# Optimization experiments

Hardware: AMD Instinct MI355X
Metric: run time of the kernel (lower is better)

The kernel has to match this reference:

```python
import jax, jax.numpy as jnp
import numpy as np

GROUP_SIZE = 64
SHARED_EXPERT_WEIGHT = 1.0
# FP4 E2M1 codebook: sign bit + {0,.5,1,1.5,2,3,4,6}
FP4_TABLE = jnp.array([0.0, 0.5, 1.0, 1.5, 2.0, 3.0, 4.0, 6.0,
                       -0.0, -0.5, -1.0, -1.5, -2.0, -3.0, -4.0, -6.0], dtype=jnp.float32)


def dequant_fp4(packed, scales, group_size=GROUP_SIZE):
    """packed: [..., K//8, N] int32 (8 nibbles along K per word),
    scales: [..., K//group_size, N] -> dequantized [..., K, N] fp32."""
    shifts = (jnp.arange(8, dtype=jnp.int32) * 4)[:, None]          # [8,1]
    nib = jnp.right_shift(packed[..., :, None, :], shifts) & 0xF     # [..., K//8, 8, N]
    w = FP4_TABLE[nib]
    K = packed.shape[-2] * 8
    w = w.reshape(packed.shape[:-2] + (K, packed.shape[-1]))         # [..., K, N]
    s = jnp.repeat(scales, group_size, axis=-2)                      # [..., K, N]
    return w * s


def setup_inputs() -> dict:
    key = jax.random.key(0)
    ks = jax.random.split(key, 12)
    T, K, I, E, TOPK = 2048, 2048, 1024, 8, 2
    GS = GROUP_SIZE
    MAXI = 2**31 - 1
    u = lambda k, shp: jax.random.uniform(k, shp, jnp.float32, 0.005, 0.02)
    probs = jax.random.uniform(ks[10], (T, TOPK), jnp.float32)
    probs = probs / probs.sum(-1, keepdims=True)
    return {
        "hidden_states": jax.random.normal(ks[0], (T, K), jnp.float32),
        "gate_up_weight_packed": jax.random.randint(ks[1], (E, K // 8, 2 * I), 0, MAXI, jnp.int32),
        "gate_up_scales": u(ks[2], (E, K // GS, 2 * I)),
        "down_weight_packed": jax.random.randint(ks[3], (E, I // 8, K), 0, MAXI, jnp.int32),
        "down_scales": u(ks[4], (E, I // GS, K)),
        "shared_gate_up_packed": jax.random.randint(ks[5], (K // 8, 2 * I), 0, MAXI, jnp.int32),
        "shared_gate_up_scales": u(ks[6], (K // GS, 2 * I)),
        "shared_down_packed": jax.random.randint(ks[7], (I // 8, K), 0, MAXI, jnp.int32),
        "shared_down_scales": u(ks[8], (I // GS, K)),
        "expert_ids": jax.random.randint(ks[9], (T, TOPK), 0, E, jnp.int32),
        "expert_probs": probs,
    }


def reference(hidden_states, gate_up_weight_packed, gate_up_scales,
              down_weight_packed, down_scales,
              shared_gate_up_packed, shared_gate_up_scales,
              shared_down_packed, shared_down_scales,
              expert_ids, expert_probs):
    x = hidden_states                                                # [T, K]
    E = gate_up_weight_packed.shape[0]
    # --- routed experts: dequant + grouped GEMM over all tokens per expert ---
    Wgu = dequant_fp4(gate_up_weight_packed, gate_up_scales)         # [E, K, 2I]
    Wd = dequant_fp4(down_weight_packed, down_scales)                # [E, I, K]
    h = jnp.einsum('tk,ekn->etn', x, Wgu)                            # [E, T, 2I]
    gate, up = jnp.split(h, 2, axis=-1)
    act = jax.nn.silu(gate) * up                                     # [E, T, I]
    y = jnp.einsum('eti,eik->etk', act, Wd)                          # [E, T, K]
    # combine[t,e] = sum over top-k slots routed to e of prob
    one_hot = jax.nn.one_hot(expert_ids, E, dtype=x.dtype)           # [T, topk, E]
    combine = jnp.einsum('tk,tke->te', expert_probs, one_hot)        # [T, E]
    out = jnp.einsum('te,etk->tk', combine, y)                       # [T, K]
    # --- shared expert (always applied, weighted) ---
    Wgu_s = dequant_fp4(shared_gate_up_packed, shared_gate_up_scales)  # [K, 2I]
    Wd_s = dequant_fp4(shared_down_packed, shared_down_scales)         # [I, K]
    hs = x @ Wgu_s
    gs, us = jnp.split(hs, 2, axis=-1)
    shared_out = (jax.nn.silu(gs) * us) @ Wd_s
    return out + SHARED_EXPERT_WEIGHT * shared_out
```

## Files before the change

### kernel.cpp

```cpp
#include <hip/hip_runtime.h>
#include <hip/hip_bf16.h>

#define T_TOK 2048
#define K_DIM 2048
#define I_DIM 1024
#define NE    8
#define TOPK  2
#define GS    64

#define NSLOT  (T_TOK * TOPK)
#define TOTROW (NSLOT + T_TOK)
#define MAXITEM 32

typedef __attribute__((ext_vector_type(8))) short short8;
typedef __attribute__((ext_vector_type(4))) float f32x4;

#define WS_XB   ((size_t)65536)
#define WS_ACT  (WS_XB  + (size_t)2048 * 2048 * 2)
#define WS_Y    (WS_ACT + (size_t)TOTROW * 1024 * 2)


__device__ __forceinline__ unsigned pack2(float a, float b) {
    __hip_bfloat162 h = __float22bfloat162_rn(make_float2(a, b));
    return *reinterpret_cast<unsigned*>(&h);
}

__device__ __forceinline__ unsigned scale2(unsigned p, float s) {
    float f0 = __uint_as_float(p << 16) * s;
    float f1 = __uint_as_float(p & 0xFFFF0000u) * s;
    return pack2(f0, f1);
}

__device__ __forceinline__ float bf2f(ushort h) {
    return __uint_as_float((unsigned)h << 16);
}

__device__ __forceinline__ void dq_word(unsigned w, float s, unsigned o[4]) {
    unsigned lo  = w & 0x0F0F0F0Fu;
    unsigned hi  = (w >> 4) & 0x0F0F0F0Fu;
    unsigned mlo = lo & 0x07070707u, mhi = hi & 0x07070707u;
    unsigned Hlo = __builtin_amdgcn_perm(0x40404040u, 0x3F3F3F00u, mlo);
    unsigned Hhi = __builtin_amdgcn_perm(0x40404040u, 0x3F3F3F00u, mhi);
    unsigned Llo = __builtin_amdgcn_perm(0xC0804000u, 0xC0800000u, mlo);
    unsigned Lhi = __builtin_amdgcn_perm(0xC0804000u, 0xC0800000u, mhi);
    Hlo |= (lo & 0x08080808u) << 4;
    Hhi |= (hi & 0x08080808u) << 4;
    unsigned e01 = __builtin_amdgcn_perm(Hlo, Llo, 0x05010400u);
    unsigned e23 = __builtin_amdgcn_perm(Hlo, Llo, 0x07030602u);
    unsigned o01 = __builtin_amdgcn_perm(Hhi, Lhi, 0x05010400u);
    unsigned o23 = __builtin_amdgcn_perm(Hhi, Lhi, 0x07030602u);
    o[0] = scale2(e01, s); o[1] = scale2(e23, s);
    o[2] = scale2(o01, s); o[3] = scale2(o23, s);
}

__device__ __forceinline__ void gld16(const void* g, void* l) {
    __builtin_amdgcn_global_load_lds(
        (const __attribute__((address_space(1))) unsigned*)g,
        (__attribute__((address_space(3))) unsigned*)l, 16, 0, 0);
}

#define PREP_BLK 2048
#define FRONT_GRID (PREP_BLK + 1)

__global__ __launch_bounds__(256) void k_front(
        const float* __restrict__ x, ushort* __restrict__ xb,
        const int* __restrict__ eids,
        int* __restrict__ gcnt, int* __restrict__ gbase,
        int* __restrict__ tileCnt, int* __restrict__ tileE, int* __restrict__ tileM,
        int* __restrict__ tok, int* __restrict__ inv) {
    int id = blockIdx.x;
    int tid = threadIdx.x;

    if (id < PREP_BLK) {
        int idx = id * 256 + tid;
        const float4* p = (const float4*)(x + (size_t)idx * 8);
        float4 f0 = p[0], f1 = p[1];
        unsigned u0 = pack2(f0.x, f0.z);
        unsigned u1 = pack2(f1.x, f1.z);
        unsigned u2 = pack2(f0.y, f0.w);
        unsigned u3 = pack2(f1.y, f1.w);
        *(int4*)(xb + (size_t)idx * 8) = make_int4(u0, u1, u2, u3);
    } else {
        __shared__ int lcnt[NE], lbase[NE], lcur[NE];
        if (tid < NE) lcnt[tid] = 0;
        __syncthreads();
        for (int i = tid; i < NSLOT; i += 256)
            atomicAdd(&lcnt[eids[i]], 1);
        __syncthreads();
        if (tid == 0) {
            int acc = 0;
            for (int e = 0; e < NE; e++) { lbase[e] = acc; acc += lcnt[e]; }
        }
        __syncthreads();
        if (tid < NE) lcur[tid] = lbase[tid];
        __syncthreads();
        for (int i = tid; i < NSLOT; i += 256) {
            int e = eids[i];
            int pos = atomicAdd(&lcur[e], 1);
            tok[pos] = i >> 1;
            inv[i] = pos;
        }
        for (int t = tid; t < T_TOK; t += 256)
            tok[NSLOT + t] = t;
        if (tid < NE) { gcnt[tid] = lcnt[tid]; gbase[tid] = lbase[tid]; }
        if (tid == 0) {
            gcnt[NE] = T_TOK; gbase[NE] = NSLOT;
            int nt = 0;
            for (int e = 0; e < NE + 1; e++) {
                int c = (e < NE) ? lcnt[e] : T_TOK;
                for (int m = 0; m < c; m += 256) { tileE[nt] = e; tileM[nt] = m; nt++; }
            }
            *tileCnt = nt;
            for (int i = nt; i < 64; i++) { tileE[i] = 0; tileM[i] = 0; }
        }
    }
}

__global__ __launch_bounds__(1024) void k_gemm_gateup(
        const ushort* __restrict__ xb,
        const int* __restrict__ gup, const float* __restrict__ gus,
        const int* __restrict__ sup, const float* __restrict__ sus,
        const int* __restrict__ gcnt, const int* __restrict__ gbase,
        const int* __restrict__ tileCnt, const int* __restrict__ tileE,
        const int* __restrict__ tileM,
        const int* __restrict__ tokid, ushort* __restrict__ act) {
    int item = blockIdx.y;
    if (item >= *tileCnt) return;
    int tid = threadIdx.x;
    int e = tileE[item], m0 = tileM[item];
    int cnt = gcnt[e], base = gbase[e];
    int n0 = blockIdx.x * 128;
    const int* wp; const float* sc;
    if (e < NE) { wp = gup + (size_t)e * 256 * 2048; sc = gus + (size_t)e * 32 * 2048; }
    else        { wp = sup; sc = sus; }

    __shared__ __align__(16) ushort xs[256 * 64];
    __shared__ __align__(16) ushort bs[256 * 64];

    int lane = tid & 63, wv = tid >> 6;
    int lid = lane & 15, quad = lane >> 4;
    int wr = wv >> 2, wc = wv & 3;
    int l8 = lane >> 3, l7 = lane & 7;
    int chunk = (l7 ^ l8) * 8;

    const ushort* aSrc[2];
    #pragma unroll
    for (int it = 0; it < 2; it++) {
        int rA = wv * 16 + it * 8 + l8;
        int t = (m0 + rA < cnt) ? tokid[base + m0 + rA] : 0;
        aSrc[it] = xb + (size_t)t * K_DIM + chunk;
    }

    int nloc = tid & 255;
    int kw0 = (tid >> 8) * 2;
    int bj = nloc & 63, bh = nloc >> 6;
    int ncol = (bj < 32) ? (n0 + bh * 32 + bj) : (I_DIM + n0 + bh * 32 + (bj - 32));
    ushort* bd0 = &bs[nloc * 64 + ((kw0    ) ^ (nloc & 7)) * 8];
    ushort* bd1 = &bs[nloc * 64 + ((kw0 + 1) ^ (nloc & 7)) * 8];

    float s   = sc[ncol];
    unsigned w0 = (unsigned)wp[(size_t)(kw0    ) * 2048 + ncol];
    unsigned w1 = (unsigned)wp[(size_t)(kw0 + 1) * 2048 + ncol];

    f32x4 acc[4][4] = {};

    for (int k0 = 0; k0 < K_DIM; k0 += 64) {
        #pragma unroll
        for (int it = 0; it < 2; it++)
            gld16(aSrc[it] + k0, &xs[(wv * 2 + it) * 512]);
        {
            unsigned o[4];
            dq_word(w0, s, o);
            *(int4*)bd0 = make_int4(o[0], o[1], o[2], o[3]);
            dq_word(w1, s, o);
            *(int4*)bd1 = make_int4(o[0], o[1], o[2], o[3]);
        }
        int kn = k0 + 64;
        if (kn < K_DIM) {
            s  = sc[(size_t)(kn >> 6) * 2048 + ncol];
            w0 = (unsigned)wp[(size_t)((kn >> 3) + kw0    ) * 2048 + ncol];
            w1 = (unsigned)wp[(size_t)((kn >> 3) + kw0 + 1) * 2048 + ncol];
        }
        __syncthreads();
        #pragma unroll
        for (int ks = 0; ks < 2; ks++) {
            int slot = ((ks * 4 + quad) ^ l7) * 8;
            short8 a[4], b[4];
            #pragma unroll
            for (int mt = 0; mt < 4; mt++)
                a[mt] = *(const short8*)&xs[(wr * 64 + mt * 16 + lid) * 64 + slot];
            #pragma unroll
            for (int nt = 0; nt < 4; nt++)
                b[nt] = *(const short8*)&bs[(wc * 64 + nt * 16 + lid) * 64 + slot];
            #pragma unroll
            for (int mt = 0; mt < 4; mt++)
                #pragma unroll
                for (int nt = 0; nt < 4; nt++)
                    acc[mt][nt] = __builtin_amdgcn_mfma_f32_16x16x32_bf16(
                        a[mt], b[nt], acc[mt][nt], 0, 0, 0);
        }
        __syncthreads();
    }

    int c7 = lid & 7;
    int delta = ((c7 >> 1) + ((c7 & 1) << 2)) - c7;
    #pragma unroll
    for (int mt = 0; mt < 4; mt++) {
        #pragma unroll
        for (int i = 0; i < 4; i++) {
            int row = wr * 64 + mt * 16 + quad * 4 + i;
            if (m0 + row < cnt) {
                size_t p = (size_t)(base + m0 + row);
                #pragma unroll
                for (int nt = 0; nt < 2; nt++) {
                    float g = acc[mt][nt][i], u = acc[mt][nt + 2][i];
                    float vv = g / (1.f + __expf(-g)) * u;
                    int ncol2 = n0 + wc * 32 + nt * 16 + lid;
                    __hip_bfloat16 hb = __float2bfloat16(vv);
                    act[p * I_DIM + ncol2 + delta] = *reinterpret_cast<ushort*>(&hb);
                }
            }
        }
    }
}

__global__ __launch_bounds__(1024) void k_gemm_down(
        const ushort* __restrict__ actb,
        const int* __restrict__ dwp, const float* __restrict__ dsc,
        const int* __restrict__ sdp, const float* __restrict__ sds,
        const int* __restrict__ gcnt, const int* __restrict__ gbase,
        const int* __restrict__ tileCnt, const int* __restrict__ tileE,
        const int* __restrict__ tileM,
        ushort* __restrict__ y) {
    int item = blockIdx.y;
    if (item >= *tileCnt) return;
    int tid = threadIdx.x;
    int e = tileE[item], m0 = tileM[item];
    int cnt = gcnt[e], base = gbase[e];
    int n0 = blockIdx.x * 256;
    const int* wp; const float* sc;
    if (e < NE) { wp = dwp + (size_t)e * 128 * 2048; sc = dsc + (size_t)e * 16 * 2048; }
    else        { wp = sdp; sc = sds; }

    __shared__ __align__(16) ushort xs[256 * 64];
    __shared__ __align__(16) ushort bs[256 * 64];

    int lane = tid & 63, wv = tid >> 6;
    int lid = lane & 15, quad = lane >> 4;
    int wr = wv >> 2, wc = wv & 3;
    int l8 = lane >> 3, l7 = lane & 7;
    int chunk = (l7 ^ l8) * 8;

    const ushort* aSrc[2];
    #pragma unroll
    for (int it = 0; it < 2; it++) {
        int rA = wv * 16 + it * 8 + l8;
        int rr = m0 + rA; if (rr >= cnt) rr = cnt - 1;
        aSrc[it] = actb + (size_t)(base + rr) * I_DIM + chunk;
    }

    int nloc = tid & 255;
    int kw0 = (tid >> 8) * 2;
    int ncol = n0 + nloc;
    ushort* bd0 = &bs[nloc * 64 + ((kw0    ) ^ (nloc & 7)) * 8];
    ushort* bd1 = &bs[nloc * 64 + ((kw0 + 1) ^ (nloc & 7)) * 8];

    float s   = sc[ncol];
    unsigned w0 = (unsigned)wp[(size_t)(kw0    ) * 2048 + ncol];
    unsigned w1 = (unsigned)wp[(size_t)(kw0 + 1) * 2048 + ncol];

    f32x4 acc[4][4] = {};

    for (int i0 = 0; i0 < I_DIM; i0 += 64) {
        #pragma unroll
        for (int it = 0; it < 2; it++)
            gld16(aSrc[it] + i0, &xs[(wv * 2 + it) * 512]);
        {
            unsigned o[4];
            dq_word(w0, s, o);
            *(int4*)bd0 = make_int4(o[0], o[1], o[2], o[3]);
            dq_word(w1, s, o);
            *(int4*)bd1 = make_int4(o[0], o[1], o[2], o[3]);
        }
        int in0 = i0 + 64;
        if (in0 < I_DIM) {
            s  = sc[(size_t)(in0 >> 6) * 2048 + ncol];
            w0 = (unsigned)wp[(size_t)((in0 >> 3) + kw0    ) * 2048 + ncol];
            w1 = (unsigned)wp[(size_t)((in0 >> 3) + kw0 + 1) * 2048 + ncol];
        }
        __syncthreads();
        #pragma unroll
        for (int ks = 0; ks < 2; ks++) {
            int slot = ((ks * 4 + quad) ^ l7) * 8;
            short8 a[4], b[4];
            #pragma unroll
            for (int mt = 0; mt < 4; mt++)
                a[mt] = *(const short8*)&xs[(wr * 64 + mt * 16 + lid) * 64 + slot];
            #pragma unroll
            for (int nt = 0; nt < 4; nt++)
                b[nt] = *(const short8*)&bs[(wc * 64 + nt * 16 + lid) * 64 + slot];
            #pragma unroll
            for (int mt = 0; mt < 4; mt++)
                #pragma unroll
                for (int nt = 0; nt < 4; nt++)
                    acc[mt][nt] = __builtin_amdgcn_mfma_f32_16x16x32_bf16(
                        a[mt], b[nt], acc[mt][nt], 0, 0, 0);
        }
        __syncthreads();
    }

    #pragma unroll
    for (int mt = 0; mt < 4; mt++) {
        #pragma unroll
        for (int i = 0; i < 4; i++) {
            int row = wr * 64 + mt * 16 + quad * 4 + i;
            if (m0 + row < cnt) {
                ushort* yrow = y + (size_t)(base + m0 + row) * 2048 + n0 + wc * 64 + lid;
                #pragma unroll
                for (int nt = 0; nt < 4; nt++) {
                    __hip_bfloat16 hb = __float2bfloat16(acc[mt][nt][i]);
                    yrow[nt * 16] = *reinterpret_cast<ushort*>(&hb);
                }
            }
        }
    }
}

__global__ __launch_bounds__(256) void k_combine(
        const ushort* __restrict__ y, const int* __restrict__ inv,
        const float* __restrict__ prb, float* __restrict__ out) {
    int idx = blockIdx.x * 256 + threadIdx.x;
    int t = idx >> 8;
    int c = (idx & 255) * 8;
    int p0 = inv[2 * t], p1 = inv[2 * t + 1];
    float w0 = prb[2 * t], w1 = prb[2 * t + 1];
    int4 a = *(const int4*)(y + (size_t)p0 * 2048 + c);
    int4 b = *(const int4*)(y + (size_t)p1 * 2048 + c);
    int4 s = *(const int4*)(y + (size_t)(NSLOT + t) * 2048 + c);
    const ushort* au = (const ushort*)&a;
    const ushort* bu = (const ushort*)&b;
    const ushort* su = (const ushort*)&s;
    float o[8];
    #pragma unroll
    for (int j = 0; j < 8; j++)
        o[j] = w0 * bf2f(au[j]) + w1 * bf2f(bu[j]) + bf2f(su[j]);
    *(float4*)(out + (size_t)t * 2048 + c)     = *(float4*)&o[0];
    *(float4*)(out + (size_t)t * 2048 + c + 4) = *(float4*)&o[4];
}

extern "C" void kernel_launch(void* const* d_in, const int* in_sizes, int n_in,
                              void* d_out, int out_size, void* d_ws, size_t ws_size,
                              hipStream_t stream) {
    const float* x    = (const float*)d_in[0];
    const int*   gup  = (const int*)d_in[1];
    const float* gus  = (const float*)d_in[2];
    const int*   dwp  = (const int*)d_in[3];
    const float* dsc  = (const float*)d_in[4];
    const int*   sup  = (const int*)d_in[5];
    const float* sus  = (const float*)d_in[6];
    const int*   sdp  = (const int*)d_in[7];
    const float* sds  = (const float*)d_in[8];
    const int*   eids = (const int*)d_in[9];
    const float* prb  = (const float*)d_in[10];
    float* out = (float*)d_out;

    char*   ws      = (char*)d_ws;
    int*    gcnt    = (int*)(ws + 0);
    int*    gbase   = (int*)(ws + 64);
    int*    tileCnt = (int*)(ws + 128);
    int*    tileE   = (int*)(ws + 192);
    int*    tileM   = (int*)(ws + 448);
    int*    tok     = (int*)(ws + 1024);
    int*    inv     = (int*)(ws + 25600);
    ushort* xb      = (ushort*)(ws + WS_XB);
    ushort* act     = (ushort*)(ws + WS_ACT);
    ushort* y       = (ushort*)(ws + WS_Y);

    k_front<<<FRONT_GRID, 256, 0, stream>>>(
        x, xb, eids, gcnt, gbase, tileCnt, tileE, tileM, tok, inv);
    k_gemm_gateup<<<dim3(I_DIM / 128, MAXITEM), 1024, 0, stream>>>(
        xb, gup, gus, sup, sus, gcnt, gbase, tileCnt, tileE, tileM, tok, act);
    k_gemm_down<<<dim3(K_DIM / 256, MAXITEM), 1024, 0, stream>>>(
        act, dwp, dsc, sdp, sds, gcnt, gbase, tileCnt, tileE, tileM, y);
    k_combine<<<(T_TOK * K_DIM / 8) / 256, 256, 0, stream>>>(y, inv, prb, out);
}
```

Before: 242.7 us.

## Double-buffer LDS tiles in gate-up and down GEMMs with one barrier per step

Result: faster. 232.4 us (-4.2%).

```diff
diff --git a/kernel.cpp b/kernel.cpp
--- a/kernel.cpp
+++ b/kernel.cpp
@@ -134,8 +134,8 @@
     if (e < NE) { wp = gup + (size_t)e * 256 * 2048; sc = gus + (size_t)e * 32 * 2048; }
     else        { wp = sup; sc = sus; }
 
-    __shared__ __align__(16) ushort xs[256 * 64];
-    __shared__ __align__(16) ushort bs[256 * 64];
+    __shared__ __align__(16) ushort xs[2][256 * 64];
+    __shared__ __align__(16) ushort bs[2][256 * 64];
 
     int lane = tid & 63, wv = tid >> 6;
     int lid = lane & 15, quad = lane >> 4;
@@ -155,43 +155,57 @@
     int kw0 = (tid >> 8) * 2;
     int bj = nloc & 63, bh = nloc >> 6;
     int ncol = (bj < 32) ? (n0 + bh * 32 + bj) : (I_DIM + n0 + bh * 32 + (bj - 32));
-    ushort* bd0 = &bs[nloc * 64 + ((kw0    ) ^ (nloc & 7)) * 8];
-    ushort* bd1 = &bs[nloc * 64 + ((kw0 + 1) ^ (nloc & 7)) * 8];
-
+    int bd0 = nloc * 64 + ((kw0    ) ^ (nloc & 7)) * 8;
+    int bd1 = nloc * 64 + ((kw0 + 1) ^ (nloc & 7)) * 8;
+
+    const int NT = K_DIM / 64;
+
+    #pragma unroll
+    for (int it = 0; it < 2; it++)
+        gld16(aSrc[it], &xs[0][(wv * 2 + it) * 512]);
     float s   = sc[ncol];
     unsigned w0 = (unsigned)wp[(size_t)(kw0    ) * 2048 + ncol];
     unsigned w1 = (unsigned)wp[(size_t)(kw0 + 1) * 2048 + ncol];
+    {
+        unsigned o[4];
+        dq_word(w0, s, o); *(int4*)&bs[0][bd0] = make_int4(o[0], o[1], o[2], o[3]);
+        dq_word(w1, s, o); *(int4*)&bs[0][bd1] = make_int4(o[0], o[1], o[2], o[3]);
+    }
+    s  = sc[(size_t)2048 + ncol];
+    w0 = (unsigned)wp[(size_t)(8 + kw0    ) * 2048 + ncol];
+    w1 = (unsigned)wp[(size_t)(8 + kw0 + 1) * 2048 + ncol];
+    __syncthreads();
 
     f32x4 acc[4][4] = {};
-
-    for (int k0 = 0; k0 < K_DIM; k0 += 64) {
-        #pragma unroll
-        for (int it = 0; it < 2; it++)
-            gld16(aSrc[it] + k0, &xs[(wv * 2 + it) * 512]);
-        {
+    int pp = 0;
+
+    #pragma unroll 2
+    for (int t = 0; t < NT; ++t) {
+        int nx = pp ^ 1;
+        if (t + 1 < NT) {
+            #pragma unroll
+            for (int it = 0; it < 2; it++)
+                gld16(aSrc[it] + (t + 1) * 64, &xs[nx][(wv * 2 + it) * 512]);
             unsigned o[4];
-            dq_word(w0, s, o);
-            *(int4*)bd0 = make_int4(o[0], o[1], o[2], o[3]);
-            dq_word(w1, s, o);
-            *(int4*)bd1 = make_int4(o[0], o[1], o[2], o[3]);
-        }
-        int kn = k0 + 64;
-        if (kn < K_DIM) {
-            s  = sc[(size_t)(kn >> 6) * 2048 + ncol];
-            w0 = (unsigned)wp[(size_t)((kn >> 3) + kw0    ) * 2048 + ncol];
-            w1 = (unsigned)wp[(size_t)((kn >> 3) + kw0 + 1) * 2048 + ncol];
-        }
-        __syncthreads();
+            dq_word(w0, s, o); *(int4*)&bs[nx][bd0] = make_int4(o[0], o[1], o[2], o[3]);
+            dq_word(w1, s, o); *(int4*)&bs[nx][bd1] = make_int4(o[0], o[1], o[2], o[3]);
+            if (t + 2 < NT) {
+                s  = sc[(size_t)(t + 2) * 2048 + ncol];
+                w0 = (unsigned)wp[(size_t)((t + 2) * 8 + kw0    ) * 2048 + ncol];
+                w1 = (unsigned)wp[(size_t)((t + 2) * 8 + kw0 + 1) * 2048 + ncol];
+            }
+        }
+        __builtin_amdgcn_s_setprio(1);
         #pragma unroll
         for (int ks = 0; ks < 2; ks++) {
             int slot = ((ks * 4 + quad) ^ l7) * 8;
             short8 a[4], b[4];
             #pragma unroll
             for (int mt = 0; mt < 4; mt++)
-                a[mt] = *(const short8*)&xs[(wr * 64 + mt * 16 + lid) * 64 + slot];
+                a[mt] = *(const short8*)&xs[pp][(wr * 64 + mt * 16 + lid) * 64 + slot];
             #pragma unroll
             for (int nt = 0; nt < 4; nt++)
-                b[nt] = *(const short8*)&bs[(wc * 64 + nt * 16 + lid) * 64 + slot];
+                b[nt] = *(const short8*)&bs[pp][(wc * 64 + nt * 16 + lid) * 64 + slot];
             #pragma unroll
             for (int mt = 0; mt < 4; mt++)
                 #pragma unroll
@@ -199,7 +213,9 @@
                     acc[mt][nt] = __builtin_amdgcn_mfma_f32_16x16x32_bf16(
                         a[mt], b[nt], acc[mt][nt], 0, 0, 0);
         }
-        __syncthreads();
+        __builtin_amdgcn_s_setprio(0);
+        __syncthreads();
+        pp = nx;
     }
 
     int c7 = lid & 7;
@@ -242,8 +258,8 @@
     if (e < NE) { wp = dwp + (size_t)e * 128 * 2048; sc = dsc + (size_t)e * 16 * 2048; }
     else        { wp = sdp; sc = sds; }
 
-    __shared__ __align__(16) ushort xs[256 * 64];
-    __shared__ __align__(16) ushort bs[256 * 64];
+    __shared__ __align__(16) ushort xs[2][256 * 64];
+    __shared__ __align__(16) ushort bs[2][256 * 64];
 
     int lane = tid & 63, wv = tid >> 6;
     int lid = lane & 15, quad = lane >> 4;
@@ -262,43 +278,57 @@
     int nloc = tid & 255;
     int kw0 = (tid >> 8) * 2;
     int ncol = n0 + nloc;
-    ushort* bd0 = &bs[nloc * 64 + ((kw0    ) ^ (nloc & 7)) * 8];
-    ushort* bd1 = &bs[nloc * 64 + ((kw0 + 1) ^ (nloc & 7)) * 8];
-
+    int bd0 = nloc * 64 + ((kw0    ) ^ (nloc & 7)) * 8;
+    int bd1 = nloc * 64 + ((kw0 + 1) ^ (nloc & 7)) * 8;
+
+    const int NT = I_DIM / 64;
+
+    #pragma unroll
+    for (int it = 0; it < 2; it++)
+        gld16(aSrc[it], &xs[0][(wv * 2 + it) * 512]);
     float s   = sc[ncol];
     unsigned w0 = (unsigned)wp[(size_t)(kw0    ) * 2048 + ncol];
     unsigned w1 = (unsigned)wp[(size_t)(kw0 + 1) * 2048 + ncol];
+    {
+        unsigned o[4];
+        dq_word(w0, s, o); *(int4*)&bs[0][bd0] = make_int4(o[0], o[1], o[2], o[3]);
+        dq_word(w1, s, o); *(int4*)&bs[0][bd1] = make_int4(o[0], o[1], o[2], o[3]);
+    }
+    s  = sc[(size_t)2048 + ncol];
+    w0 = (unsigned)wp[(size_t)(8 + kw0    ) * 2048 + ncol];
+    w1 = (unsigned)wp[(size_t)(8 + kw0 + 1) * 2048 + ncol];
+    __syncthreads();
 
     f32x4 acc[4][4] = {};
-
-    for (int i0 = 0; i0 < I_DIM; i0 += 64) {
-        #pragma unroll
-        for (int it = 0; it < 2; it++)
-            gld16(aSrc[it] + i0, &xs[(wv * 2 + it) * 512]);
-        {
+    int pp = 0;
+
+    #pragma unroll 2
+    for (int t = 0; t < NT; ++t) {
+        int nx = pp ^ 1;
+        if (t + 1 < NT) {
+            #pragma unroll
+            for (int it = 0; it < 2; it++)
+                gld16(aSrc[it] + (t + 1) * 64, &xs[nx][(wv * 2 + it) * 512]);
             unsigned o[4];
-            dq_word(w0, s, o);
-            *(int4*)bd0 = make_int4(o[0], o[1], o[2], o[3]);
-            dq_word(w1, s, o);
-            *(int4*)bd1 = make_int4(o[0], o[1], o[2], o[3]);
-        }
-        int in0 = i0 + 64;
-        if (in0 < I_DIM) {
-            s  = sc[(size_t)(in0 >> 6) * 2048 + ncol];
-            w0 = (unsigned)wp[(size_t)((in0 >> 3) + kw0    ) * 2048 + ncol];
-            w1 = (unsigned)wp[(size_t)((in0 >> 3) + kw0 + 1) * 2048 + ncol];
-        }
-        __syncthreads();
+            dq_word(w0, s, o); *(int4*)&bs[nx][bd0] = make_int4(o[0], o[1], o[2], o[3]);
+            dq_word(w1, s, o); *(int4*)&bs[nx][bd1] = make_int4(o[0], o[1], o[2], o[3]);
+            if (t + 2 < NT) {
+                s  = sc[(size_t)(t + 2) * 2048 + ncol];
+                w0 = (unsigned)wp[(size_t)((t + 2) * 8 + kw0    ) * 2048 + ncol];
+                w1 = (unsigned)wp[(size_t)((t + 2) * 8 + kw0 + 1) * 2048 + ncol];
+            }
+        }
+        __builtin_amdgcn_s_setprio(1);
         #pragma unroll
         for (int ks = 0; ks < 2; ks++) {
             int slot = ((ks * 4 + quad) ^ l7) * 8;
             short8 a[4], b[4];
             #pragma unroll
             for (int mt = 0; mt < 4; mt++)
-                a[mt] = *(const short8*)&xs[(wr * 64 + mt * 16 + lid) * 64 + slot];
+                a[mt] = *(const short8*)&xs[pp][(wr * 64 + mt * 16 + lid) * 64 + slot];
             #pragma unroll
             for (int nt = 0; nt < 4; nt++)
-                b[nt] = *(const short8*)&bs[(wc * 64 + nt * 16 + lid) * 64 + slot];
+                b[nt] = *(const short8*)&bs[pp][(wc * 64 + nt * 16 + lid) * 64 + slot];
             #pragma unroll
             for (int mt = 0; mt < 4; mt++)
                 #pragma unroll
@@ -306,7 +336,9 @@
                     acc[mt][nt] = __builtin_amdgcn_mfma_f32_16x16x32_bf16(
                         a[mt], b[nt], acc[mt][nt], 0, 0, 0);
         }
-        __syncthreads();
+        __builtin_amdgcn_s_setprio(0);
+        __syncthreads();
+        pp = nx;
     }
 
     #pragma unroll
```

## Halve GEMM N-tile and block size, add MFMA priority and pointer-increment loads

Applied to the files above, without the earlier changes.

Result: faster. 228.5 us (-5.9%).

```diff
diff --git a/kernel.cpp b/kernel.cpp
--- a/kernel.cpp
+++ b/kernel.cpp
@@ -116,7 +116,7 @@
     }
 }
 
-__global__ __launch_bounds__(1024) void k_gemm_gateup(
+__global__ __launch_bounds__(512) void k_gemm_gateup(
         const ushort* __restrict__ xb,
         const int* __restrict__ gup, const float* __restrict__ gus,
         const int* __restrict__ sup, const float* __restrict__ sus,
@@ -129,59 +129,64 @@
     int tid = threadIdx.x;
     int e = tileE[item], m0 = tileM[item];
     int cnt = gcnt[e], base = gbase[e];
-    int n0 = blockIdx.x * 128;
+    int n0 = blockIdx.x * 64;
     const int* wp; const float* sc;
     if (e < NE) { wp = gup + (size_t)e * 256 * 2048; sc = gus + (size_t)e * 32 * 2048; }
     else        { wp = sup; sc = sus; }
 
     __shared__ __align__(16) ushort xs[256 * 64];
-    __shared__ __align__(16) ushort bs[256 * 64];
+    __shared__ __align__(16) ushort bs[128 * 64];
 
     int lane = tid & 63, wv = tid >> 6;
     int lid = lane & 15, quad = lane >> 4;
-    int wr = wv >> 2, wc = wv & 3;
+    int wr = wv >> 1, wc = wv & 1;
     int l8 = lane >> 3, l7 = lane & 7;
     int chunk = (l7 ^ l8) * 8;
 
-    const ushort* aSrc[2];
-    #pragma unroll
-    for (int it = 0; it < 2; it++) {
-        int rA = wv * 16 + it * 8 + l8;
+    const ushort* aSrc[4];
+    #pragma unroll
+    for (int it = 0; it < 4; it++) {
+        int rA = wv * 32 + it * 8 + l8;
         int t = (m0 + rA < cnt) ? tokid[base + m0 + rA] : 0;
         aSrc[it] = xb + (size_t)t * K_DIM + chunk;
     }
 
-    int nloc = tid & 255;
-    int kw0 = (tid >> 8) * 2;
+    int nloc = tid & 127;
+    int kw0 = (tid >> 7) * 2;
     int bj = nloc & 63, bh = nloc >> 6;
     int ncol = (bj < 32) ? (n0 + bh * 32 + bj) : (I_DIM + n0 + bh * 32 + (bj - 32));
-    ushort* bd0 = &bs[nloc * 64 + ((kw0    ) ^ (nloc & 7)) * 8];
-    ushort* bd1 = &bs[nloc * 64 + ((kw0 + 1) ^ (nloc & 7)) * 8];
-
-    float s   = sc[ncol];
-    unsigned w0 = (unsigned)wp[(size_t)(kw0    ) * 2048 + ncol];
-    unsigned w1 = (unsigned)wp[(size_t)(kw0 + 1) * 2048 + ncol];
+    int bd0 = nloc * 64 + ((kw0    ) ^ (nloc & 7)) * 8;
+    int bd1 = nloc * 64 + ((kw0 + 1) ^ (nloc & 7)) * 8;
+
+    const int NT = K_DIM / 64;
+    const int* wq = wp + (size_t)kw0 * 2048 + ncol;
+    const float* sq = sc + ncol;
+    unsigned w0 = (unsigned)wq[0];
+    unsigned w1 = (unsigned)wq[2048];
+    float s = *sq;
+    wq += 16384; sq += 2048;
 
     f32x4 acc[4][4] = {};
 
-    for (int k0 = 0; k0 < K_DIM; k0 += 64) {
-        #pragma unroll
-        for (int it = 0; it < 2; it++)
-            gld16(aSrc[it] + k0, &xs[(wv * 2 + it) * 512]);
+    for (int t = 0; t < NT; ++t) {
+        #pragma unroll
+        for (int it = 0; it < 4; it++) {
+            gld16(aSrc[it], &xs[(wv * 4 + it) * 512]);
+            aSrc[it] += 64;
+        }
         {
             unsigned o[4];
-            dq_word(w0, s, o);
-            *(int4*)bd0 = make_int4(o[0], o[1], o[2], o[3]);
-            dq_word(w1, s, o);
-            *(int4*)bd1 = make_int4(o[0], o[1], o[2], o[3]);
-        }
-        int kn = k0 + 64;
-        if (kn < K_DIM) {
-            s  = sc[(size_t)(kn >> 6) * 2048 + ncol];
-            w0 = (unsigned)wp[(size_t)((kn >> 3) + kw0    ) * 2048 + ncol];
-            w1 = (unsigned)wp[(size_t)((kn >> 3) + kw0 + 1) * 2048 + ncol];
-        }
-        __syncthreads();
+            dq_word(w0, s, o); *(int4*)&bs[bd0] = make_int4(o[0], o[1], o[2], o[3]);
+            dq_word(w1, s, o); *(int4*)&bs[bd1] = make_int4(o[0], o[1], o[2], o[3]);
+        }
+        if (t + 1 < NT) {
+            w0 = (unsigned)wq[0];
+            w1 = (unsigned)wq[2048];
+            s = *sq;
+            wq += 16384; sq += 2048;
+        }
+        __syncthreads();
+        __builtin_amdgcn_s_setprio(1);
         #pragma unroll
         for (int ks = 0; ks < 2; ks++) {
             int slot = ((ks * 4 + quad) ^ l7) * 8;
@@ -199,6 +204,7 @@
                     acc[mt][nt] = __builtin_amdgcn_mfma_f32_16x16x32_bf16(
                         a[mt], b[nt], acc[mt][nt], 0, 0, 0);
         }
+        __builtin_amdgcn_s_setprio(0);
         __syncthreads();
     }
 
@@ -224,7 +230,7 @@
     }
 }
 
-__global__ __launch_bounds__(1024) void k_gemm_down(
+__global__ __launch_bounds__(512) void k_gemm_down(
         const ushort* __restrict__ actb,
         const int* __restrict__ dwp, const float* __restrict__ dsc,
         const int* __restrict__ sdp, const float* __restrict__ sds,
@@ -237,58 +243,63 @@
     int tid = threadIdx.x;
     int e = tileE[item], m0 = tileM[item];
     int cnt = gcnt[e], base = gbase[e];
-    int n0 = blockIdx.x * 256;
+    int n0 = blockIdx.x * 128;
     const int* wp; const float* sc;
     if (e < NE) { wp = dwp + (size_t)e * 128 * 2048; sc = dsc + (size_t)e * 16 * 2048; }
     else        { wp = sdp; sc = sds; }
 
     __shared__ __align__(16) ushort xs[256 * 64];
-    __shared__ __align__(16) ushort bs[256 * 64];
+    __shared__ __align__(16) ushort bs[128 * 64];
 
     int lane = tid & 63, wv = tid >> 6;
     int lid = lane & 15, quad = lane >> 4;
-    int wr = wv >> 2, wc = wv & 3;
+    int wr = wv >> 1, wc = wv & 1;
     int l8 = lane >> 3, l7 = lane & 7;
     int chunk = (l7 ^ l8) * 8;
 
-    const ushort* aSrc[2];
-    #pragma unroll
-    for (int it = 0; it < 2; it++) {
-        int rA = wv * 16 + it * 8 + l8;
+    const ushort* aSrc[4];
+    #pragma unroll
+    for (int it = 0; it < 4; it++) {
+        int rA = wv * 32 + it * 8 + l8;
         int rr = m0 + rA; if (rr >= cnt) rr = cnt - 1;
         aSrc[it] = actb + (size_t)(base + rr) * I_DIM + chunk;
     }
 
-    int nloc = tid & 255;
-    int kw0 = (tid >> 8) * 2;
+    int nloc = tid & 127;
+    int kw0 = (tid >> 7) * 2;
     int ncol = n0 + nloc;
-    ushort* bd0 = &bs[nloc * 64 + ((kw0    ) ^ (nloc & 7)) * 8];
-    ushort* bd1 = &bs[nloc * 64 + ((kw0 + 1) ^ (nloc & 7)) * 8];
-
-    float s   = sc[ncol];
-    unsigned w0 = (unsigned)wp[(size_t)(kw0    ) * 2048 + ncol];
-    unsigned w1 = (unsigned)wp[(size_t)(kw0 + 1) * 2048 + ncol];
+    int bd0 = nloc * 64 + ((kw0    ) ^ (nloc & 7)) * 8;
+    int bd1 = nloc * 64 + ((kw0 + 1) ^ (nloc & 7)) * 8;
+
+    const int NT = I_DIM / 64;
+    const int* wq = wp + (size_t)kw0 * 2048 + ncol;
+    const float* sq = sc + ncol;
+    unsigned w0 = (unsigned)wq[0];
+    unsigned w1 = (unsigned)wq[2048];
+    float s = *sq;
+    wq += 16384; sq += 2048;
 
     f32x4 acc[4][4] = {};
 
-    for (int i0 = 0; i0 < I_DIM; i0 += 64) {
-        #pragma unroll
-        for (int it = 0; it < 2; it++)
-            gld16(aSrc[it] + i0, &xs[(wv * 2 + it) * 512]);
+    for (int t = 0; t < NT; ++t) {
+        #pragma unroll
+        for (int it = 0; it < 4; it++) {
+            gld16(aSrc[it], &xs[(wv * 4 + it) * 512]);
+            aSrc[it] += 64;
+        }
         {
             unsigned o[4];
-            dq_word(w0, s, o);
-            *(int4*)bd0 = make_int4(o[0], o[1], o[2], o[3]);
-            dq_word(w1, s, o);
-            *(int4*)bd1 = make_int4(o[0], o[1], o[2], o[3]);
-        }
-        int in0 = i0 + 64;
-        if (in0 < I_DIM) {
-            s  = sc[(size_t)(in0 >> 6) * 2048 + ncol];
-            w0 = (unsigned)wp[(size_t)((in0 >> 3) + kw0    ) * 2048 + ncol];
-            w1 = (unsigned)wp[(size_t)((in0 >> 3) + kw0 + 1) * 2048 + ncol];
-        }
-        __syncthreads();
+            dq_word(w0, s, o); *(int4*)&bs[bd0] = make_int4(o[0], o[1], o[2], o[3]);
+            dq_word(w1, s, o); *(int4*)&bs[bd1] = make_int4(o[0], o[1], o[2], o[3]);
+        }
+        if (t + 1 < NT) {
+            w0 = (unsigned)wq[0];
+            w1 = (unsigned)wq[2048];
+            s = *sq;
+            wq += 16384; sq += 2048;
+        }
+        __syncthreads();
+        __builtin_amdgcn_s_setprio(1);
         #pragma unroll
         for (int ks = 0; ks < 2; ks++) {
             int slot = ((ks * 4 + quad) ^ l7) * 8;
@@ -306,6 +317,7 @@
                     acc[mt][nt] = __builtin_amdgcn_mfma_f32_16x16x32_bf16(
                         a[mt], b[nt], acc[mt][nt], 0, 0, 0);
         }
+        __builtin_amdgcn_s_setprio(0);
         __syncthreads();
     }
 
@@ -378,9 +390,9 @@
 
     k_front<<<FRONT_GRID, 256, 0, stream>>>(
         x, xb, eids, gcnt, gbase, tileCnt, tileE, tileM, tok, inv);
-    k_gemm_gateup<<<dim3(I_DIM / 128, MAXITEM), 1024, 0, stream>>>(
+    k_gemm_gateup<<<dim3(I_DIM / 64, MAXITEM), 512, 0, stream>>>(
         xb, gup, gus, sup, sus, gcnt, gbase, tileCnt, tileE, tileM, tok, act);
-    k_gemm_down<<<dim3(K_DIM / 256, MAXITEM), 1024, 0, stream>>>(
+    k_gemm_down<<<dim3(K_DIM / 128, MAXITEM), 512, 0, stream>>>(
         act, dwp, dsc, sdp, sds, gcnt, gbase, tileCnt, tileE, tileM, y);
     k_combine<<<(T_TOK * K_DIM / 8) / 256, 256, 0, stream>>>(y, inv, prb, out);
 }
```
